# Optimization experiments

Measured on AMD Instinct MI355X. Metric: run time of the kernel, lower is better.

Reference implementation:

```python
import jax, jax.numpy as jnp
import numpy as np

N_EMBD = 1024
N_HEAD = 16
HEAD_DIM = N_EMBD // N_HEAD


def setup_inputs() -> dict:
    key = jax.random.key(0)
    k1, k2, k3 = jax.random.split(key, 3)
    x = jax.random.normal(k1, (4, 2048, N_EMBD), dtype=jnp.float32)
    w_qkv = jax.random.normal(k2, (N_EMBD, 3 * N_EMBD), dtype=jnp.float32) * (N_EMBD ** -0.5)
    w_proj = jax.random.normal(k3, (N_EMBD, N_EMBD), dtype=jnp.float32) * (N_EMBD ** -0.5)
    return {"x": x, "w_qkv": w_qkv, "w_proj": w_proj}


def reference(x, w_qkv, w_proj):
    B, T, C = x.shape
    qkv = jnp.einsum('btc,cd->btd', x, w_qkv)  # [B,T,3C]
    q, k, v = jnp.split(qkv, 3, axis=-1)
    def heads(t):
        return t.reshape(B, T, N_HEAD, HEAD_DIM).transpose(0, 2, 1, 3)  # [B,H,T,D]
    q, k, v = heads(q), heads(k), heads(v)
    scale = 1.0 / jnp.sqrt(jnp.asarray(HEAD_DIM, dtype=x.dtype))
    att = jnp.einsum('bhqd,bhkd->bhqk', q, k) * scale  # [B,H,T,T]
    causal = jnp.tril(jnp.ones((T, T), dtype=bool))
    att = jnp.where(causal[None, None], att, jnp.asarray(-jnp.inf, dtype=att.dtype))
    att = jax.nn.softmax(att, axis=-1)
    out = jnp.einsum('bhqk,bhkd->bhqd', att, v)  # [B,H,T,D]
    out = out.transpose(0, 2, 1, 3).reshape(B, T, C)
    return jnp.einsum('btc,cd->btd', out, w_proj)
```

## Files before the change

### kernel.cpp

```cpp
#include <hip/hip_runtime.h>
#include <cstdint>
#include <cstddef>
#include <type_traits>

typedef float  f32x4    __attribute__((ext_vector_type(4)));
typedef __bf16 bf16x8   __attribute__((ext_vector_type(8)));
typedef short  short4_t __attribute__((ext_vector_type(4)));
typedef short  short8_t __attribute__((ext_vector_type(8)));

__device__ __forceinline__ short f2bf(float f) {
  return __builtin_bit_cast(short, (__bf16)f);
}

__global__ void transpose_bf16(const float* __restrict__ W, short* __restrict__ WT,
                               int K, int N) {
  __shared__ float tile[32][33];
  int tx = threadIdx.x & 31, ty = threadIdx.x >> 5;
  int n0 = blockIdx.x * 32, k0 = blockIdx.y * 32;
#pragma unroll
  for (int i = 0; i < 32; i += 8)
    tile[ty + i][tx] = W[(size_t)(k0 + ty + i) * N + n0 + tx];
  __syncthreads();
#pragma unroll
  for (int i = 0; i < 32; i += 8)
    WT[(size_t)(n0 + ty + i) * K + k0 + tx] = f2bf(tile[tx][ty + i]);
}

template <int MODE, bool AF32>
__global__ __launch_bounds__(256, 2) void gemm_bt(
    const void* __restrict__ Av, const short* __restrict__ Bt,
    float* __restrict__ outf, short* __restrict__ Qo, short* __restrict__ Ko,
    short* __restrict__ Vo, int M, int N, int K) {
  constexpr int SMEM = (MODE == 1) ? (128 * 136 * 2) : 16384;
  __shared__ alignas(16) char smem[SMEM];
  short* As = (short*)smem;
  short* Bs = (short*)(smem + 8192);

  const int tid = threadIdx.x;
  const int lane = tid & 63, wave = tid >> 6;
  const int g = lane & 15, q = lane >> 4;
  const int m0 = blockIdx.y * 128, n0 = blockIdx.x * 128;
  const int wm = (wave >> 1) * 64, wn = (wave & 1) * 64;

  const int srow = tid >> 2;
  const int scol = (tid & 3) * 8;
  const float* Af = (const float*)Av;
  const short* Ab = (const short*)Av;

  f32x4    raf[4];
  short8_t ra[2], rb[2];

  auto load_regs = [&](int k0) {
    if constexpr (AF32) {
      const float* p0 = &Af[(size_t)(m0 + srow) * K + k0 + scol];
      const float* p1 = &Af[(size_t)(m0 + 64 + srow) * K + k0 + scol];
      raf[0] = *(const f32x4*)p0; raf[1] = *(const f32x4*)(p0 + 4);
      raf[2] = *(const f32x4*)p1; raf[3] = *(const f32x4*)(p1 + 4);
    } else {
      ra[0] = *(const short8_t*)&Ab[(size_t)(m0 + srow) * K + k0 + scol];
      ra[1] = *(const short8_t*)&Ab[(size_t)(m0 + 64 + srow) * K + k0 + scol];
    }
    rb[0] = *(const short8_t*)&Bt[(size_t)(n0 + srow) * K + k0 + scol];
    rb[1] = *(const short8_t*)&Bt[(size_t)(n0 + 64 + srow) * K + k0 + scol];
  };
  auto store_regs = [&]() {
    short8_t w0, w1;
    if constexpr (AF32) {
#pragma unroll
      for (int j = 0; j < 4; j++) {
        w0[j] = f2bf(raf[0][j]); w0[4 + j] = f2bf(raf[1][j]);
        w1[j] = f2bf(raf[2][j]); w1[4 + j] = f2bf(raf[3][j]);
      }
    } else { w0 = ra[0]; w1 = ra[1]; }
    *(short8_t*)&As[tid * 8] = w0;
    *(short8_t*)&As[(tid + 256) * 8] = w1;
    *(short8_t*)&Bs[tid * 8] = rb[0];
    *(short8_t*)&Bs[(tid + 256) * 8] = rb[1];
  };

  f32x4 acc[4][4] = {};
  const int KB = K >> 5;
  load_regs(0);
  for (int kb = 0; kb < KB; kb++) {
    __syncthreads();
    store_regs();
    if (kb + 1 < KB) load_regs((kb + 1) << 5);
    __syncthreads();
    bf16x8 af[4], bfr[4];
#pragma unroll
    for (int mt = 0; mt < 4; mt++)
      af[mt] = *(const bf16x8*)&As[(wm + mt * 16 + g) * 32 + q * 8];
#pragma unroll
    for (int nt = 0; nt < 4; nt++)
      bfr[nt] = *(const bf16x8*)&Bs[(wn + nt * 16 + g) * 32 + q * 8];
#pragma unroll
    for (int mt = 0; mt < 4; mt++)
#pragma unroll
      for (int nt = 0; nt < 4; nt++)
        acc[mt][nt] = __builtin_amdgcn_mfma_f32_16x16x32_bf16(af[mt], bfr[nt],
                                                              acc[mt][nt], 0, 0, 0);
  }

  if (MODE == 0) {
#pragma unroll
    for (int mt = 0; mt < 4; mt++)
#pragma unroll
      for (int nt = 0; nt < 4; nt++) {
        int n = n0 + wn + nt * 16 + g;
        int mbase = m0 + wm + mt * 16 + q * 4;
#pragma unroll
        for (int r = 0; r < 4; r++)
          outf[(size_t)(mbase + r) * N + n] = acc[mt][nt][r];
      }
  } else {
    const int which = n0 >> 10;
    const int b = m0 >> 11;
    if (which == 2) {
#pragma unroll
      for (int nt = 0; nt < 4; nt++) {
        int c = (n0 + wn + nt * 16 + g) & 1023;
        int h = c >> 6, d = c & 63;
#pragma unroll
        for (int mt = 0; mt < 4; mt++) {
          int t = (m0 + wm + mt * 16 + q * 4) & 2047;
          short4_t pv;
#pragma unroll
          for (int r = 0; r < 4; r++) pv[r] = f2bf(acc[mt][nt][r]);
          *(short4_t*)&Vo[((size_t)((b << 4) + h) * 64 + d) * 2048 + t] = pv;
        }
      }
    } else {
      __syncthreads();
      short* Cs = (short*)smem;
#pragma unroll
      for (int mt = 0; mt < 4; mt++)
#pragma unroll
        for (int nt = 0; nt < 4; nt++)
#pragma unroll
          for (int r = 0; r < 4; r++)
            Cs[(wm + mt * 16 + q * 4 + r) * 136 + wn + nt * 16 + g] =
                f2bf(acc[mt][nt][r]);
      __syncthreads();
      short* dst = (which == 0) ? Qo : Ko;
      const int h0 = (n0 & 1023) >> 6;
      const int trow = tid >> 1, half = tid & 1;
      const int t = (m0 + trow) & 2047;
      const size_t gb = ((size_t)((b << 4) + h0 + half) * 2048 + t) * 64;
#pragma unroll
      for (int j = 0; j < 8; j++)
        *(short8_t*)&dst[gb + j * 8] =
            *(const short8_t*)&Cs[trow * 136 + half * 64 + j * 8];
    }
  }
}

__global__ __launch_bounds__(256, 2) void attn_fwd(
    const short* __restrict__ Qg, const short* __restrict__ Kg,
    const short* __restrict__ Vt, short* __restrict__ Og) {
  __shared__ alignas(16) short Ks[128 * 72];
  __shared__ alignas(16) short VTs[64 * 136];
  __shared__ alignas(16) short Ps[4][32 * 72];

  const int tid = threadIdx.x, lane = tid & 63, wave = tid >> 6;
  const int g = lane & 15, q = lane >> 4;
  const int id = blockIdx.x;
  const int bh = id & 63;
  const int qt = 15 - (id >> 6);
  const size_t base = (size_t)bh * (2048 * 64);
  const int b = bh >> 4, h = bh & 15;
  const float cs = 0.18033688011f;

  bf16x8 bq[2][2];
  {
    const short* Qp = Qg + base + (size_t)qt * 128 * 64;
#pragma unroll
    for (int nt = 0; nt < 2; nt++)
#pragma unroll
      for (int kk = 0; kk < 2; kk++) {
        bf16x8 v = *(const bf16x8*)&Qp[(wave * 32 + nt * 16 + g) * 64 + kk * 32 + q * 8];
#pragma unroll
        for (int j = 0; j < 8; j++) v[j] = (__bf16)((float)v[j] * cs);
        bq[nt][kk] = v;
      }
  }

  short8_t kreg[4], vreg[4];
  auto loadKV = [&](int kt) {
    const short* Kp  = Kg + base + (size_t)kt * 128 * 64;
    const short* Vtp = Vt + base + (size_t)kt * 128;
#pragma unroll
    for (int i = 0; i < 4; i++) {
      int c = tid + i * 256;
      kreg[i] = *(const short8_t*)&Kp[(c >> 3) * 64 + (c & 7) * 8];
      vreg[i] = *(const short8_t*)&Vtp[(size_t)(c >> 4) * 2048 + (c & 15) * 8];
    }
  };
  auto storeKV = [&]() {
#pragma unroll
    for (int i = 0; i < 4; i++) {
      int c = tid + i * 256;
      *(short8_t*)&Ks[(c >> 3) * 72 + (c & 7) * 8] = kreg[i];
      *(short8_t*)&VTs[(c >> 4) * 136 + (c & 15) * 8] = vreg[i];
    }
  };

  f32x4 ot[4][2] = {};
  float m_run[2] = {-1e30f, -1e30f};
  float l_run[2] = {0.0f, 0.0f};

  auto compute = [&](auto diagc) {
    constexpr bool DIAG = decltype(diagc)::value;
    f32x4 st[8][2] = {};
#pragma unroll
    for (int kk = 0; kk < 2; kk++)
#pragma unroll
      for (int mt = 0; mt < 8; mt++) {
        bf16x8 ak = *(const bf16x8*)&Ks[(mt * 16 + g) * 72 + kk * 32 + q * 8];
#pragma unroll
        for (int nt = 0; nt < 2; nt++)
          st[mt][nt] = __builtin_amdgcn_mfma_f32_16x16x32_bf16(ak, bq[nt][kk],
                                                               st[mt][nt], 0, 0, 0);
      }

    float mnew[2], alpha[2], psum[2];
#pragma unroll
    for (int nt = 0; nt < 2; nt++) {
      const int qloc = wave * 32 + nt * 16 + g;
      float tmax = -1e30f;
#pragma unroll
      for (int mt = 0; mt < 8; mt++)
#pragma unroll
        for (int r = 0; r < 4; r++) {
          if (DIAG) {
            if (mt * 16 + q * 4 + r > qloc) st[mt][nt][r] = -1e30f;
          }
          tmax = fmaxf(tmax, st[mt][nt][r]);
        }
      tmax = fmaxf(tmax, __shfl_xor(tmax, 16));
      tmax = fmaxf(tmax, __shfl_xor(tmax, 32));
      mnew[nt] = fmaxf(m_run[nt], tmax);
      alpha[nt] = __builtin_amdgcn_exp2f(m_run[nt] - mnew[nt]);
      m_run[nt] = mnew[nt];
      psum[nt] = 0.0f;
#pragma unroll
      for (int mt = 0; mt < 4; mt++) {
        ot[mt][nt][0] *= alpha[nt]; ot[mt][nt][1] *= alpha[nt];
        ot[mt][nt][2] *= alpha[nt]; ot[mt][nt][3] *= alpha[nt];
      }
    }

    short* Pw = &Ps[wave][0];
#pragma unroll
    for (int half = 0; half < 2; half++) {
#pragma unroll
      for (int nt = 0; nt < 2; nt++)
#pragma unroll
        for (int mh = 0; mh < 4; mh++) {
          const int mt = half * 4 + mh;
          short4_t pk4;
#pragma unroll
          for (int r = 0; r < 4; r++) {
            float p = __builtin_amdgcn_exp2f(st[mt][nt][r] - mnew[nt]);
            psum[nt] += p;
            pk4[r] = f2bf(p);
          }
          *(short4_t*)&Pw[(nt * 16 + g) * 72 + mh * 16 + q * 4] = pk4;
        }
#pragma unroll
      for (int kh = 0; kh < 2; kh++) {
        const int kk = half * 2 + kh;
        bf16x8 pb[2];
#pragma unroll
        for (int nt = 0; nt < 2; nt++)
          pb[nt] = *(const bf16x8*)&Pw[(nt * 16 + g) * 72 + kh * 32 + q * 8];
#pragma unroll
        for (int mt = 0; mt < 4; mt++) {
          bf16x8 av = *(const bf16x8*)&VTs[(mt * 16 + g) * 136 + kk * 32 + q * 8];
#pragma unroll
          for (int nt = 0; nt < 2; nt++)
            ot[mt][nt] = __builtin_amdgcn_mfma_f32_16x16x32_bf16(av, pb[nt],
                                                                 ot[mt][nt], 0, 0, 0);
        }
      }
    }

#pragma unroll
    for (int nt = 0; nt < 2; nt++) {
      float ps = psum[nt];
      ps += __shfl_xor(ps, 16);
      ps += __shfl_xor(ps, 32);
      l_run[nt] = l_run[nt] * alpha[nt] + ps;
    }
  };

  loadKV(0);
  for (int kt = 0; kt < qt; kt++) {
    __syncthreads();
    storeKV();
    loadKV(kt + 1);
    __syncthreads();
    compute(std::integral_constant<bool, false>{});
  }
  __syncthreads();
  storeKV();
  __syncthreads();
  compute(std::integral_constant<bool, true>{});

#pragma unroll
  for (int nt = 0; nt < 2; nt++) {
    const float inv = 1.0f / l_run[nt];
    const int qrow = qt * 128 + wave * 32 + nt * 16 + g;
    size_t obase = ((size_t)b * 2048 + qrow) * 1024 + h * 64;
#pragma unroll
    for (int mt = 0; mt < 4; mt++) {
      short4_t ov;
#pragma unroll
      for (int r = 0; r < 4; r++) ov[r] = f2bf(ot[mt][nt][r] * inv);
      *(short4_t*)&Og[obase + mt * 16 + q * 4] = ov;
    }
  }
}

extern "C" void kernel_launch(void* const* d_in, const int* in_sizes, int n_in,
                              void* d_out, int out_size, void* d_ws, size_t ws_size,
                              hipStream_t stream) {
  const float* x      = (const float*)d_in[0];
  const float* w_qkv  = (const float*)d_in[1];
  const float* w_proj = (const float*)d_in[2];
  float* out = (float*)d_out;

  char* ws = (char*)d_ws;
  short* wqkvT  = (short*)(ws);
  short* wprojT = (short*)(ws + 6291456);
  short* Qb     = (short*)(ws + 8388608);
  short* Kb     = (short*)(ws + 25165824);
  short* Vtb    = (short*)(ws + 41943040);
  short* Ob     = (short*)(ws + 58720256);

  {
    dim3 gq(96, 32); transpose_bf16<<<gq, 256, 0, stream>>>(w_qkv, wqkvT, 1024, 3072);
    dim3 gp(32, 32); transpose_bf16<<<gp, 256, 0, stream>>>(w_proj, wprojT, 1024, 1024);
  }
  {
    dim3 g(24, 64);
    gemm_bt<1, true><<<g, 256, 0, stream>>>(x, wqkvT, nullptr, Qb, Kb, Vtb,
                                            8192, 3072, 1024);
  }
  {
    attn_fwd<<<dim3(1024), 256, 0, stream>>>(Qb, Kb, Vtb, Ob);
  }
  {
    dim3 g(8, 64);
    gemm_bt<0, false><<<g, 256, 0, stream>>>(Ob, wprojT, out, nullptr, nullptr,
                                             nullptr, 8192, 1024, 1024);
  }
}
```

Baseline: 264.5 us.

## Widen QKV GEMM tile, split attention softmax into sub-blocks, raise occupancy

```diff
diff --git a/kernel.cpp b/kernel.cpp
--- a/kernel.cpp
+++ b/kernel.cpp
@@ -26,54 +26,133 @@
     WT[(size_t)(n0 + ty + i) * K + k0 + tx] = f2bf(tile[tx][ty + i]);
 }
 
-template <int MODE, bool AF32>
-__global__ __launch_bounds__(256, 2) void gemm_bt(
-    const void* __restrict__ Av, const short* __restrict__ Bt,
-    float* __restrict__ outf, short* __restrict__ Qo, short* __restrict__ Ko,
-    short* __restrict__ Vo, int M, int N, int K) {
-  constexpr int SMEM = (MODE == 1) ? (128 * 136 * 2) : 16384;
-  __shared__ alignas(16) char smem[SMEM];
+__global__ __launch_bounds__(256, 2) void gemm_qkv(
+    const float* __restrict__ Af, const short* __restrict__ Bt,
+    short* __restrict__ Qo, short* __restrict__ Ko, short* __restrict__ Vo) {
+  constexpr int K = 1024;
+  __shared__ alignas(16) char smem[34816];
   short* As = (short*)smem;
   short* Bs = (short*)(smem + 8192);
-
+  short* Cs = (short*)smem;
+
+  const int tid = threadIdx.x;
+  const int lane = tid & 63, wave = tid >> 6;
+  const int g = lane & 15, q = lane >> 4;
+  const int n0 = blockIdx.x * 256, m0 = blockIdx.y * 128;
+  const int wm = (wave >> 1) * 64, wn = (wave & 1) * 128;
+
+  const int arow = tid >> 1, acol = (tid & 1) * 16;
+  const float* ap = &Af[(size_t)(m0 + arow) * K + acol];
+  const short* bp = &Bt[(size_t)(n0 + tid) * K];
+
+  f32x4    raf[4];
+  short8_t rb[4];
+  auto load_regs = [&](int k0) {
+#pragma unroll
+    for (int j = 0; j < 4; j++) raf[j] = *(const f32x4*)(ap + k0 + j * 4);
+#pragma unroll
+    for (int j = 0; j < 4; j++) rb[j] = *(const short8_t*)(bp + k0 + j * 8);
+  };
+  auto store_regs = [&]() {
+    short8_t w0, w1;
+#pragma unroll
+    for (int j = 0; j < 4; j++) {
+      w0[j] = f2bf(raf[0][j]); w0[4 + j] = f2bf(raf[1][j]);
+      w1[j] = f2bf(raf[2][j]); w1[4 + j] = f2bf(raf[3][j]);
+    }
+    *(short8_t*)&As[arow * 32 + acol]     = w0;
+    *(short8_t*)&As[arow * 32 + acol + 8] = w1;
+#pragma unroll
+    for (int j = 0; j < 4; j++) *(short8_t*)&Bs[tid * 32 + j * 8] = rb[j];
+  };
+
+  f32x4 acc[4][8] = {};
+  load_regs(0);
+  for (int kb = 0; kb < K / 32; kb++) {
+    __syncthreads();
+    store_regs();
+    if (kb + 1 < K / 32) load_regs((kb + 1) * 32);
+    __syncthreads();
+    bf16x8 af[4];
+#pragma unroll
+    for (int mt = 0; mt < 4; mt++)
+      af[mt] = *(const bf16x8*)&As[(wm + mt * 16 + g) * 32 + q * 8];
+#pragma unroll
+    for (int nt = 0; nt < 8; nt++) {
+      bf16x8 bfr = *(const bf16x8*)&Bs[(wn + nt * 16 + g) * 32 + q * 8];
+#pragma unroll
+      for (int mt = 0; mt < 4; mt++)
+        acc[mt][nt] = __builtin_amdgcn_mfma_f32_16x16x32_bf16(af[mt], bfr,
+                                                              acc[mt][nt], 0, 0, 0);
+    }
+  }
+
+  const int which = n0 >> 10;
+  const int b = m0 >> 11;
+  if (which == 2) {
+#pragma unroll
+    for (int nt = 0; nt < 8; nt++) {
+      int c = (n0 + wn + nt * 16 + g) & 1023;
+      int h = c >> 6, d = c & 63;
+#pragma unroll
+      for (int mt = 0; mt < 4; mt++) {
+        int t = (m0 + wm + mt * 16 + q * 4) & 2047;
+        short4_t pv;
+#pragma unroll
+        for (int r = 0; r < 4; r++) pv[r] = f2bf(acc[mt][nt][r]);
+        *(short4_t*)&Vo[((size_t)((b << 4) + h) * 64 + d) * 2048 + t] = pv;
+      }
+    }
+  } else {
+    short* dst = (which == 0) ? Qo : Ko;
+#pragma unroll
+    for (int ch = 0; ch < 2; ch++) {
+      __syncthreads();
+      if ((wave & 1) == ch) {
+#pragma unroll
+        for (int mt = 0; mt < 4; mt++)
+#pragma unroll
+          for (int nt = 0; nt < 8; nt++)
+#pragma unroll
+            for (int r = 0; r < 4; r++)
+              Cs[(wm + mt * 16 + q * 4 + r) * 136 + nt * 16 + g] =
+                  f2bf(acc[mt][nt][r]);
+      }
+      __syncthreads();
+      const int h0 = ((n0 + ch * 128) & 1023) >> 6;
+      const int trow = tid >> 1, half = tid & 1;
+      const int t = (m0 + trow) & 2047;
+      const size_t gb = ((size_t)((b << 4) + h0 + half) * 2048 + t) * 64;
+#pragma unroll
+      for (int j = 0; j < 8; j++)
+        *(short8_t*)&dst[gb + j * 8] =
+            *(const short8_t*)&Cs[trow * 136 + half * 64 + j * 8];
+    }
+  }
+}
+
+__global__ __launch_bounds__(256, 2) void gemm_proj(
+    const short* __restrict__ Ab, const short* __restrict__ Bt,
+    float* __restrict__ outf, int M, int N, int K) {
+  __shared__ alignas(16) short As[128 * 32];
+  __shared__ alignas(16) short Bs[128 * 32];
   const int tid = threadIdx.x;
   const int lane = tid & 63, wave = tid >> 6;
   const int g = lane & 15, q = lane >> 4;
   const int m0 = blockIdx.y * 128, n0 = blockIdx.x * 128;
   const int wm = (wave >> 1) * 64, wn = (wave & 1) * 64;
 
-  const int srow = tid >> 2;
-  const int scol = (tid & 3) * 8;
-  const float* Af = (const float*)Av;
-  const short* Ab = (const short*)Av;
-
-  f32x4    raf[4];
+  const int srow = tid >> 2, scol = (tid & 3) * 8;
   short8_t ra[2], rb[2];
-
   auto load_regs = [&](int k0) {
-    if constexpr (AF32) {
-      const float* p0 = &Af[(size_t)(m0 + srow) * K + k0 + scol];
-      const float* p1 = &Af[(size_t)(m0 + 64 + srow) * K + k0 + scol];
-      raf[0] = *(const f32x4*)p0; raf[1] = *(const f32x4*)(p0 + 4);
-      raf[2] = *(const f32x4*)p1; raf[3] = *(const f32x4*)(p1 + 4);
-    } else {
-      ra[0] = *(const short8_t*)&Ab[(size_t)(m0 + srow) * K + k0 + scol];
-      ra[1] = *(const short8_t*)&Ab[(size_t)(m0 + 64 + srow) * K + k0 + scol];
-    }
+    ra[0] = *(const short8_t*)&Ab[(size_t)(m0 + srow) * K + k0 + scol];
+    ra[1] = *(const short8_t*)&Ab[(size_t)(m0 + 64 + srow) * K + k0 + scol];
     rb[0] = *(const short8_t*)&Bt[(size_t)(n0 + srow) * K + k0 + scol];
     rb[1] = *(const short8_t*)&Bt[(size_t)(n0 + 64 + srow) * K + k0 + scol];
   };
   auto store_regs = [&]() {
-    short8_t w0, w1;
-    if constexpr (AF32) {
-#pragma unroll
-      for (int j = 0; j < 4; j++) {
-        w0[j] = f2bf(raf[0][j]); w0[4 + j] = f2bf(raf[1][j]);
-        w1[j] = f2bf(raf[2][j]); w1[4 + j] = f2bf(raf[3][j]);
-      }
-    } else { w0 = ra[0]; w1 = ra[1]; }
-    *(short8_t*)&As[tid * 8] = w0;
-    *(short8_t*)&As[(tid + 256) * 8] = w1;
+    *(short8_t*)&As[tid * 8] = ra[0];
+    *(short8_t*)&As[(tid + 256) * 8] = ra[1];
     *(short8_t*)&Bs[tid * 8] = rb[0];
     *(short8_t*)&Bs[(tid + 256) * 8] = rb[1];
   };
@@ -100,61 +179,19 @@
         acc[mt][nt] = __builtin_amdgcn_mfma_f32_16x16x32_bf16(af[mt], bfr[nt],
                                                               acc[mt][nt], 0, 0, 0);
   }
-
-  if (MODE == 0) {
-#pragma unroll
-    for (int mt = 0; mt < 4; mt++)
-#pragma unroll
-      for (int nt = 0; nt < 4; nt++) {
-        int n = n0 + wn + nt * 16 + g;
-        int mbase = m0 + wm + mt * 16 + q * 4;
-#pragma unroll
-        for (int r = 0; r < 4; r++)
-          outf[(size_t)(mbase + r) * N + n] = acc[mt][nt][r];
-      }
-  } else {
-    const int which = n0 >> 10;
-    const int b = m0 >> 11;
-    if (which == 2) {
-#pragma unroll
-      for (int nt = 0; nt < 4; nt++) {
-        int c = (n0 + wn + nt * 16 + g) & 1023;
-        int h = c >> 6, d = c & 63;
-#pragma unroll
-        for (int mt = 0; mt < 4; mt++) {
-          int t = (m0 + wm + mt * 16 + q * 4) & 2047;
-          short4_t pv;
-#pragma unroll
-          for (int r = 0; r < 4; r++) pv[r] = f2bf(acc[mt][nt][r]);
-          *(short4_t*)&Vo[((size_t)((b << 4) + h) * 64 + d) * 2048 + t] = pv;
-        }
-      }
-    } else {
-      __syncthreads();
-      short* Cs = (short*)smem;
-#pragma unroll
-      for (int mt = 0; mt < 4; mt++)
-#pragma unroll
-        for (int nt = 0; nt < 4; nt++)
-#pragma unroll
-          for (int r = 0; r < 4; r++)
-            Cs[(wm + mt * 16 + q * 4 + r) * 136 + wn + nt * 16 + g] =
-                f2bf(acc[mt][nt][r]);
-      __syncthreads();
-      short* dst = (which == 0) ? Qo : Ko;
-      const int h0 = (n0 & 1023) >> 6;
-      const int trow = tid >> 1, half = tid & 1;
-      const int t = (m0 + trow) & 2047;
-      const size_t gb = ((size_t)((b << 4) + h0 + half) * 2048 + t) * 64;
-#pragma unroll
-      for (int j = 0; j < 8; j++)
-        *(short8_t*)&dst[gb + j * 8] =
-            *(const short8_t*)&Cs[trow * 136 + half * 64 + j * 8];
-    }
-  }
-}
-
-__global__ __launch_bounds__(256, 2) void attn_fwd(
+#pragma unroll
+  for (int mt = 0; mt < 4; mt++)
+#pragma unroll
+    for (int nt = 0; nt < 4; nt++) {
+      int n = n0 + wn + nt * 16 + g;
+      int mbase = m0 + wm + mt * 16 + q * 4;
+#pragma unroll
+      for (int r = 0; r < 4; r++)
+        outf[(size_t)(mbase + r) * N + n] = acc[mt][nt][r];
+    }
+}
+
+__global__ __launch_bounds__(256, 3) void attn_fwd(
     const short* __restrict__ Qg, const short* __restrict__ Kg,
     const short* __restrict__ Vt, short* __restrict__ Og) {
   __shared__ alignas(16) short Ks[128 * 72];
@@ -207,56 +244,51 @@
   f32x4 ot[4][2] = {};
   float m_run[2] = {-1e30f, -1e30f};
   float l_run[2] = {0.0f, 0.0f};
+  short* Pw = &Ps[wave][0];
 
   auto compute = [&](auto diagc) {
     constexpr bool DIAG = decltype(diagc)::value;
-    f32x4 st[8][2] = {};
-#pragma unroll
-    for (int kk = 0; kk < 2; kk++)
-#pragma unroll
-      for (int mt = 0; mt < 8; mt++) {
-        bf16x8 ak = *(const bf16x8*)&Ks[(mt * 16 + g) * 72 + kk * 32 + q * 8];
-#pragma unroll
-        for (int nt = 0; nt < 2; nt++)
-          st[mt][nt] = __builtin_amdgcn_mfma_f32_16x16x32_bf16(ak, bq[nt][kk],
-                                                               st[mt][nt], 0, 0, 0);
-      }
-
-    float mnew[2], alpha[2], psum[2];
-#pragma unroll
-    for (int nt = 0; nt < 2; nt++) {
-      const int qloc = wave * 32 + nt * 16 + g;
-      float tmax = -1e30f;
-#pragma unroll
-      for (int mt = 0; mt < 8; mt++)
-#pragma unroll
-        for (int r = 0; r < 4; r++) {
-          if (DIAG) {
-            if (mt * 16 + q * 4 + r > qloc) st[mt][nt][r] = -1e30f;
+#pragma unroll
+    for (int sub = 0; sub < 2; sub++) {
+      f32x4 st[4][2] = {};
+#pragma unroll
+      for (int kk = 0; kk < 2; kk++)
+#pragma unroll
+        for (int mt = 0; mt < 4; mt++) {
+          bf16x8 ak = *(const bf16x8*)&Ks[(sub * 64 + mt * 16 + g) * 72 + kk * 32 + q * 8];
+#pragma unroll
+          for (int nt = 0; nt < 2; nt++)
+            st[mt][nt] = __builtin_amdgcn_mfma_f32_16x16x32_bf16(ak, bq[nt][kk],
+                                                                 st[mt][nt], 0, 0, 0);
+        }
+
+      float mnew[2], alpha[2], psum[2];
+#pragma unroll
+      for (int nt = 0; nt < 2; nt++) {
+        const int qloc = wave * 32 + nt * 16 + g;
+        float tmax = -1e30f;
+#pragma unroll
+        for (int mt = 0; mt < 4; mt++)
+#pragma unroll
+          for (int r = 0; r < 4; r++) {
+            if (DIAG) {
+              if (sub * 64 + mt * 16 + q * 4 + r > qloc) st[mt][nt][r] = -1e30f;
+            }
+            tmax = fmaxf(tmax, st[mt][nt][r]);
           }
-          tmax = fmaxf(tmax, st[mt][nt][r]);
+        tmax = fmaxf(tmax, __shfl_xor(tmax, 16));
+        tmax = fmaxf(tmax, __shfl_xor(tmax, 32));
+        mnew[nt] = fmaxf(m_run[nt], tmax);
+        alpha[nt] = __builtin_amdgcn_exp2f(m_run[nt] - mnew[nt]);
+        m_run[nt] = mnew[nt];
+        psum[nt] = 0.0f;
+#pragma unroll
+        for (int mt = 0; mt < 4; mt++) {
+          ot[mt][nt][0] *= alpha[nt]; ot[mt][nt][1] *= alpha[nt];
+          ot[mt][nt][2] *= alpha[nt]; ot[mt][nt][3] *= alpha[nt];
         }
-      tmax = fmaxf(tmax, __shfl_xor(tmax, 16));
-      tmax = fmaxf(tmax, __shfl_xor(tmax, 32));
-      mnew[nt] = fmaxf(m_run[nt], tmax);
-      alpha[nt] = __builtin_amdgcn_exp2f(m_run[nt] - mnew[nt]);
-      m_run[nt] = mnew[nt];
-      psum[nt] = 0.0f;
-#pragma unroll
-      for (int mt = 0; mt < 4; mt++) {
-        ot[mt][nt][0] *= alpha[nt]; ot[mt][nt][1] *= alpha[nt];
-        ot[mt][nt][2] *= alpha[nt]; ot[mt][nt][3] *= alpha[nt];
-      }
-    }
-
-    short* Pw = &Ps[wave][0];
-#pragma unroll
-    for (int half = 0; half < 2; half++) {
-#pragma unroll
-      for (int nt = 0; nt < 2; nt++)
-#pragma unroll
-        for (int mh = 0; mh < 4; mh++) {
-          const int mt = half * 4 + mh;
+#pragma unroll
+        for (int mt = 0; mt < 4; mt++) {
           short4_t pk4;
 #pragma unroll
           for (int r = 0; r < 4; r++) {
@@ -264,32 +296,33 @@
             psum[nt] += p;
             pk4[r] = f2bf(p);
           }
-          *(short4_t*)&Pw[(nt * 16 + g) * 72 + mh * 16 + q * 4] = pk4;
+          *(short4_t*)&Pw[(nt * 16 + g) * 72 + mt * 16 + q * 4] = pk4;
         }
+      }
+
 #pragma unroll
       for (int kh = 0; kh < 2; kh++) {
-        const int kk = half * 2 + kh;
         bf16x8 pb[2];
 #pragma unroll
         for (int nt = 0; nt < 2; nt++)
           pb[nt] = *(const bf16x8*)&Pw[(nt * 16 + g) * 72 + kh * 32 + q * 8];
 #pragma unroll
         for (int mt = 0; mt < 4; mt++) {
-          bf16x8 av = *(const bf16x8*)&VTs[(mt * 16 + g) * 136 + kk * 32 + q * 8];
+          bf16x8 av = *(const bf16x8*)&VTs[(mt * 16 + g) * 136 + sub * 64 + kh * 32 + q * 8];
 #pragma unroll
           for (int nt = 0; nt < 2; nt++)
             ot[mt][nt] = __builtin_amdgcn_mfma_f32_16x16x32_bf16(av, pb[nt],
                                                                  ot[mt][nt], 0, 0, 0);
         }
       }
-    }
-
-#pragma unroll
-    for (int nt = 0; nt < 2; nt++) {
-      float ps = psum[nt];
-      ps += __shfl_xor(ps, 16);
-      ps += __shfl_xor(ps, 32);
-      l_run[nt] = l_run[nt] * alpha[nt] + ps;
+
+#pragma unroll
+      for (int nt = 0; nt < 2; nt++) {
+        float ps = psum[nt];
+        ps += __shfl_xor(ps, 16);
+        ps += __shfl_xor(ps, 32);
+        l_run[nt] = l_run[nt] * alpha[nt] + ps;
+      }
     }
   };
 
@@ -342,16 +375,14 @@
     dim3 gp(32, 32); transpose_bf16<<<gp, 256, 0, stream>>>(w_proj, wprojT, 1024, 1024);
   }
   {
-    dim3 g(24, 64);
-    gemm_bt<1, true><<<g, 256, 0, stream>>>(x, wqkvT, nullptr, Qb, Kb, Vtb,
-                                            8192, 3072, 1024);
+    dim3 g(12, 64);
+    gemm_qkv<<<g, 256, 0, stream>>>(x, wqkvT, Qb, Kb, Vtb);
   }
   {
     attn_fwd<<<dim3(1024), 256, 0, stream>>>(Qb, Kb, Vtb, Ob);
   }
   {
     dim3 g(8, 64);
-    gemm_bt<0, false><<<g, 256, 0, stream>>>(Ob, wprojT, out, nullptr, nullptr,
-                                             nullptr, 8192, 1024, 1024);
-  }
-}
+    gemm_proj<<<g, 256, 0, stream>>>(Ob, wprojT, out, 8192, 1024, 1024);
+  }
+}
```

After: 363.3 us. +37.4%, slower.

## Double GEMM K-tile to 64 with padded LDS and split attention softmax into 64-key halves

Applied to the files above, without the earlier changes.

```diff
diff --git a/kernel.cpp b/kernel.cpp
--- a/kernel.cpp
+++ b/kernel.cpp
@@ -31,10 +31,10 @@
     const void* __restrict__ Av, const short* __restrict__ Bt,
     float* __restrict__ outf, short* __restrict__ Qo, short* __restrict__ Ko,
     short* __restrict__ Vo, int M, int N, int K) {
-  constexpr int SMEM = (MODE == 1) ? (128 * 136 * 2) : 16384;
-  __shared__ alignas(16) char smem[SMEM];
+  __shared__ alignas(16) char smem[36864];
   short* As = (short*)smem;
-  short* Bs = (short*)(smem + 8192);
+  short* Bs = (short*)(smem + 18432);
+  short* Cs = (short*)smem;
 
   const int tid = threadIdx.x;
   const int lane = tid & 63, wave = tid >> 6;
@@ -42,63 +42,67 @@
   const int m0 = blockIdx.y * 128, n0 = blockIdx.x * 128;
   const int wm = (wave >> 1) * 64, wn = (wave & 1) * 64;
 
-  const int srow = tid >> 2;
-  const int scol = (tid & 3) * 8;
+  const int srow = tid >> 1;
+  const int scol = (tid & 1) * 32;
   const float* Af = (const float*)Av;
   const short* Ab = (const short*)Av;
-
-  f32x4    raf[4];
-  short8_t ra[2], rb[2];
+  const float* ap  = &Af[(size_t)(m0 + srow) * K + scol];
+  const short* abp = &Ab[(size_t)(m0 + srow) * K + scol];
+  const short* bp  = &Bt[(size_t)(n0 + srow) * K + scol];
+
+  f32x4    raf[8];
+  short8_t ra[4], rb[4];
 
   auto load_regs = [&](int k0) {
     if constexpr (AF32) {
-      const float* p0 = &Af[(size_t)(m0 + srow) * K + k0 + scol];
-      const float* p1 = &Af[(size_t)(m0 + 64 + srow) * K + k0 + scol];
-      raf[0] = *(const f32x4*)p0; raf[1] = *(const f32x4*)(p0 + 4);
-      raf[2] = *(const f32x4*)p1; raf[3] = *(const f32x4*)(p1 + 4);
+#pragma unroll
+      for (int j = 0; j < 8; j++) raf[j] = *(const f32x4*)(ap + k0 + j * 4);
     } else {
-      ra[0] = *(const short8_t*)&Ab[(size_t)(m0 + srow) * K + k0 + scol];
-      ra[1] = *(const short8_t*)&Ab[(size_t)(m0 + 64 + srow) * K + k0 + scol];
-    }
-    rb[0] = *(const short8_t*)&Bt[(size_t)(n0 + srow) * K + k0 + scol];
-    rb[1] = *(const short8_t*)&Bt[(size_t)(n0 + 64 + srow) * K + k0 + scol];
+#pragma unroll
+      for (int j = 0; j < 4; j++) ra[j] = *(const short8_t*)(abp + k0 + j * 8);
+    }
+#pragma unroll
+    for (int j = 0; j < 4; j++) rb[j] = *(const short8_t*)(bp + k0 + j * 8);
   };
   auto store_regs = [&]() {
-    short8_t w0, w1;
-    if constexpr (AF32) {
-#pragma unroll
-      for (int j = 0; j < 4; j++) {
-        w0[j] = f2bf(raf[0][j]); w0[4 + j] = f2bf(raf[1][j]);
-        w1[j] = f2bf(raf[2][j]); w1[4 + j] = f2bf(raf[3][j]);
-      }
-    } else { w0 = ra[0]; w1 = ra[1]; }
-    *(short8_t*)&As[tid * 8] = w0;
-    *(short8_t*)&As[(tid + 256) * 8] = w1;
-    *(short8_t*)&Bs[tid * 8] = rb[0];
-    *(short8_t*)&Bs[(tid + 256) * 8] = rb[1];
+#pragma unroll
+    for (int j = 0; j < 4; j++) {
+      short8_t w;
+      if constexpr (AF32) {
+#pragma unroll
+        for (int i = 0; i < 4; i++) {
+          w[i] = f2bf(raf[2 * j][i]); w[4 + i] = f2bf(raf[2 * j + 1][i]);
+        }
+      } else w = ra[j];
+      *(short8_t*)&As[srow * 72 + scol + j * 8] = w;
+      *(short8_t*)&Bs[srow * 72 + scol + j * 8] = rb[j];
+    }
   };
 
   f32x4 acc[4][4] = {};
-  const int KB = K >> 5;
+  const int KB = K >> 6;
   load_regs(0);
   for (int kb = 0; kb < KB; kb++) {
     __syncthreads();
     store_regs();
-    if (kb + 1 < KB) load_regs((kb + 1) << 5);
+    if (kb + 1 < KB) load_regs((kb + 1) << 6);
     __syncthreads();
-    bf16x8 af[4], bfr[4];
-#pragma unroll
-    for (int mt = 0; mt < 4; mt++)
-      af[mt] = *(const bf16x8*)&As[(wm + mt * 16 + g) * 32 + q * 8];
-#pragma unroll
-    for (int nt = 0; nt < 4; nt++)
-      bfr[nt] = *(const bf16x8*)&Bs[(wn + nt * 16 + g) * 32 + q * 8];
-#pragma unroll
-    for (int mt = 0; mt < 4; mt++)
+#pragma unroll
+    for (int kk = 0; kk < 2; kk++) {
+      bf16x8 af[4], bfr[4];
+#pragma unroll
+      for (int mt = 0; mt < 4; mt++)
+        af[mt] = *(const bf16x8*)&As[(wm + mt * 16 + g) * 72 + kk * 32 + q * 8];
 #pragma unroll
       for (int nt = 0; nt < 4; nt++)
-        acc[mt][nt] = __builtin_amdgcn_mfma_f32_16x16x32_bf16(af[mt], bfr[nt],
-                                                              acc[mt][nt], 0, 0, 0);
+        bfr[nt] = *(const bf16x8*)&Bs[(wn + nt * 16 + g) * 72 + kk * 32 + q * 8];
+#pragma unroll
+      for (int mt = 0; mt < 4; mt++)
+#pragma unroll
+        for (int nt = 0; nt < 4; nt++)
+          acc[mt][nt] = __builtin_amdgcn_mfma_f32_16x16x32_bf16(af[mt], bfr[nt],
+                                                                acc[mt][nt], 0, 0, 0);
+    }
   }
 
   if (MODE == 0) {
@@ -131,7 +135,6 @@
       }
     } else {
       __syncthreads();
-      short* Cs = (short*)smem;
 #pragma unroll
       for (int mt = 0; mt < 4; mt++)
 #pragma unroll
@@ -207,56 +210,51 @@
   f32x4 ot[4][2] = {};
   float m_run[2] = {-1e30f, -1e30f};
   float l_run[2] = {0.0f, 0.0f};
+  short* Pw = &Ps[wave][0];
 
   auto compute = [&](auto diagc) {
     constexpr bool DIAG = decltype(diagc)::value;
-    f32x4 st[8][2] = {};
-#pragma unroll
-    for (int kk = 0; kk < 2; kk++)
-#pragma unroll
-      for (int mt = 0; mt < 8; mt++) {
-        bf16x8 ak = *(const bf16x8*)&Ks[(mt * 16 + g) * 72 + kk * 32 + q * 8];
-#pragma unroll
-        for (int nt = 0; nt < 2; nt++)
-          st[mt][nt] = __builtin_amdgcn_mfma_f32_16x16x32_bf16(ak, bq[nt][kk],
-                                                               st[mt][nt], 0, 0, 0);
-      }
-
-    float mnew[2], alpha[2], psum[2];
-#pragma unroll
-    for (int nt = 0; nt < 2; nt++) {
-      const int qloc = wave * 32 + nt * 16 + g;
-      float tmax = -1e30f;
-#pragma unroll
-      for (int mt = 0; mt < 8; mt++)
-#pragma unroll
-        for (int r = 0; r < 4; r++) {
-          if (DIAG) {
-            if (mt * 16 + q * 4 + r > qloc) st[mt][nt][r] = -1e30f;
+#pragma unroll
+    for (int sub = 0; sub < 2; sub++) {
+      f32x4 st[4][2] = {};
+#pragma unroll
+      for (int kk = 0; kk < 2; kk++)
+#pragma unroll
+        for (int mt = 0; mt < 4; mt++) {
+          bf16x8 ak = *(const bf16x8*)&Ks[(sub * 64 + mt * 16 + g) * 72 + kk * 32 + q * 8];
+#pragma unroll
+          for (int nt = 0; nt < 2; nt++)
+            st[mt][nt] = __builtin_amdgcn_mfma_f32_16x16x32_bf16(ak, bq[nt][kk],
+                                                                 st[mt][nt], 0, 0, 0);
+        }
+
+      float mnew[2], alpha[2], psum[2];
+#pragma unroll
+      for (int nt = 0; nt < 2; nt++) {
+        const int qloc = wave * 32 + nt * 16 + g;
+        float tmax = -1e30f;
+#pragma unroll
+        for (int mt = 0; mt < 4; mt++)
+#pragma unroll
+          for (int r = 0; r < 4; r++) {
+            if (DIAG) {
+              if (sub * 64 + mt * 16 + q * 4 + r > qloc) st[mt][nt][r] = -1e30f;
+            }
+            tmax = fmaxf(tmax, st[mt][nt][r]);
           }
-          tmax = fmaxf(tmax, st[mt][nt][r]);
-        }
-      tmax = fmaxf(tmax, __shfl_xor(tmax, 16));
-      tmax = fmaxf(tmax, __shfl_xor(tmax, 32));
-      mnew[nt] = fmaxf(m_run[nt], tmax);
-      alpha[nt] = __builtin_amdgcn_exp2f(m_run[nt] - mnew[nt]);
-      m_run[nt] = mnew[nt];
-      psum[nt] = 0.0f;
-#pragma unroll
-      for (int mt = 0; mt < 4; mt++) {
-        ot[mt][nt][0] *= alpha[nt]; ot[mt][nt][1] *= alpha[nt];
-        ot[mt][nt][2] *= alpha[nt]; ot[mt][nt][3] *= alpha[nt];
-      }
-    }
-
-    short* Pw = &Ps[wave][0];
-#pragma unroll
-    for (int half = 0; half < 2; half++) {
-#pragma unroll
-      for (int nt = 0; nt < 2; nt++)
-#pragma unroll
-        for (int mh = 0; mh < 4; mh++) {
-          const int mt = half * 4 + mh;
+        tmax = fmaxf(tmax, __shfl_xor(tmax, 16));
+        tmax = fmaxf(tmax, __shfl_xor(tmax, 32));
+        mnew[nt] = fmaxf(m_run[nt], tmax);
+        alpha[nt] = __builtin_amdgcn_exp2f(m_run[nt] - mnew[nt]);
+        m_run[nt] = mnew[nt];
+        psum[nt] = 0.0f;
+#pragma unroll
+        for (int mt = 0; mt < 4; mt++) {
+          ot[mt][nt][0] *= alpha[nt]; ot[mt][nt][1] *= alpha[nt];
+          ot[mt][nt][2] *= alpha[nt]; ot[mt][nt][3] *= alpha[nt];
+        }
+#pragma unroll
+        for (int mt = 0; mt < 4; mt++) {
           short4_t pk4;
 #pragma unroll
           for (int r = 0; r < 4; r++) {
@@ -264,32 +262,33 @@
             psum[nt] += p;
             pk4[r] = f2bf(p);
           }
-          *(short4_t*)&Pw[(nt * 16 + g) * 72 + mh * 16 + q * 4] = pk4;
-        }
+          *(short4_t*)&Pw[(nt * 16 + g) * 72 + mt * 16 + q * 4] = pk4;
+        }
+      }
+
 #pragma unroll
       for (int kh = 0; kh < 2; kh++) {
-        const int kk = half * 2 + kh;
         bf16x8 pb[2];
 #pragma unroll
         for (int nt = 0; nt < 2; nt++)
           pb[nt] = *(const bf16x8*)&Pw[(nt * 16 + g) * 72 + kh * 32 + q * 8];
 #pragma unroll
         for (int mt = 0; mt < 4; mt++) {
-          bf16x8 av = *(const bf16x8*)&VTs[(mt * 16 + g) * 136 + kk * 32 + q * 8];
+          bf16x8 av = *(const bf16x8*)&VTs[(mt * 16 + g) * 136 + sub * 64 + kh * 32 + q * 8];
 #pragma unroll
           for (int nt = 0; nt < 2; nt++)
             ot[mt][nt] = __builtin_amdgcn_mfma_f32_16x16x32_bf16(av, pb[nt],
                                                                  ot[mt][nt], 0, 0, 0);
         }
       }
-    }
-
-#pragma unroll
-    for (int nt = 0; nt < 2; nt++) {
-      float ps = psum[nt];
-      ps += __shfl_xor(ps, 16);
-      ps += __shfl_xor(ps, 32);
-      l_run[nt] = l_run[nt] * alpha[nt] + ps;
+
+#pragma unroll
+      for (int nt = 0; nt < 2; nt++) {
+        float ps = psum[nt];
+        ps += __shfl_xor(ps, 16);
+        ps += __shfl_xor(ps, 32);
+        l_run[nt] = l_run[nt] * alpha[nt] + ps;
+      }
     }
   };
 
```

Result: slower. 309.2 us (+16.9%).
